# Kernel tuning notes

Measured on AMD Instinct MI355X. Metric: run time of the kernel, lower is better.

The kernel has to match this reference:

```python
import jax, jax.numpy as jnp
import numpy as np

B, S, F = 8, 2048, 256
NUM_HEADS, HEAD_DIM = 8, 64
PROJ = NUM_HEADS * HEAD_DIM


def setup_inputs() -> dict:
    key = jax.random.key(0)
    ks = jax.random.split(key, 5)
    scale = 1.0 / np.sqrt(F)
    return {
        "x": jax.random.normal(ks[0], (B, S, F), dtype=jnp.float32),
        "Wq": jax.random.normal(ks[1], (F, PROJ), dtype=jnp.float32) * scale,
        "Wk": jax.random.normal(ks[2], (F, PROJ), dtype=jnp.float32) * scale,
        "Wv": jax.random.normal(ks[3], (F, PROJ), dtype=jnp.float32) * scale,
        "Wo": jax.random.normal(ks[4], (PROJ, F), dtype=jnp.float32) * (1.0 / np.sqrt(PROJ)),
        "bo": jnp.zeros((F,), dtype=jnp.float32),
    }


def _split_heads(t):
    # [B, S, PROJ] -> [B, H, S, D]
    b, s, _ = t.shape
    return t.reshape(b, s, NUM_HEADS, HEAD_DIM).transpose(0, 2, 1, 3)


def reference(x, Wq, Wk, Wv, Wo, bo):
    q = _split_heads(x @ Wq)  # [B,H,S,D]
    k = _split_heads(x @ Wk)
    v = _split_heads(x @ Wv)

    scale = jnp.sqrt(jnp.asarray(HEAD_DIM, dtype=x.dtype))
    score = jnp.einsum("bhqd,bhkd->bhqk", q, k) / scale  # [B,H,S,S]

    # additive causal mask: -1e9 above the diagonal (matches tf band_part trick)
    s = x.shape[1]
    neg = (1.0 - jnp.tril(jnp.ones((s, s), dtype=x.dtype))) * -1e9
    score = score + neg[None, None, :, :]

    weights = jax.nn.softmax(score, axis=-1)
    attn = jnp.einsum("bhqk,bhkd->bhqd", weights, v)  # [B,H,S,D]
    concat = attn.transpose(0, 2, 1, 3).reshape(x.shape[0], s, PROJ)
    out = concat @ Wo + bo  # [B,S,F]
    return out[:, -1, :]  # keep only last sequence position
```

## Files before the change

kernel.cpp:

```cpp
#include <hip/hip_runtime.h>

#define BB 8
#define SS 2048
#define FF 256
#define HH 8
#define DD 64
#define PROJ 512
#define NCHUNK 32
#define CHUNK (SS / NCHUNK)

__global__ void __launch_bounds__(256) k_qr(
    const float* __restrict__ x, const float* __restrict__ Wq,
    const float* __restrict__ Wk, float* __restrict__ r) {
    const int b = blockIdx.x / HH;
    const int h = blockIdx.x % HH;
    const int t = threadIdx.x;
    __shared__ float xrow[FF];
    __shared__ float qp[4][DD];
    __shared__ float qh[DD];

    xrow[t] = x[((size_t)b * SS + (SS - 1)) * FF + t];
    __syncthreads();

    {
        const int g = t >> 6, d = t & 63;
        float acc = 0.f;
        const float* wqp = Wq + (size_t)(g * 64) * PROJ + h * DD + d;
#pragma unroll 8
        for (int j = 0; j < 64; ++j)
            acc += xrow[g * 64 + j] * wqp[(size_t)j * PROJ];
        qp[g][d] = acc;
    }
    __syncthreads();
    if (t < DD) qh[t] = qp[0][t] + qp[1][t] + qp[2][t] + qp[3][t];
    __syncthreads();

    const float4* wk4 = reinterpret_cast<const float4*>(Wk + (size_t)t * PROJ + h * DD);
    float acc = 0.f;
#pragma unroll
    for (int d4 = 0; d4 < DD / 4; ++d4) {
        float4 w = wk4[d4];
        acc += w.x * qh[d4 * 4 + 0] + w.y * qh[d4 * 4 + 1] +
               w.z * qh[d4 * 4 + 2] + w.w * qh[d4 * 4 + 3];
    }
    r[(size_t)blockIdx.x * FF + t] = acc * 0.125f;
}

__global__ void __launch_bounds__(512) k_chunks(
    const float* __restrict__ x, const float* __restrict__ r,
    float* __restrict__ ycp, float* __restrict__ lpart) {
    const int b = blockIdx.x / NCHUNK;
    const int c = blockIdx.x % NCHUNK;
    const int t = threadIdx.x;
    __shared__ float rl[HH][FF + 4];
    __shared__ float es[HH][CHUNK + 4];
    __shared__ float yp[2][HH][FF];

    for (int i = t; i < HH * FF; i += 512)
        rl[i >> 8][i & 255] = r[(size_t)b * HH * FF + i];
    __syncthreads();

    {
        const int sl = t >> 3, h = t & 7;
        const float4* xp = reinterpret_cast<const float4*>(
            x + ((size_t)b * SS + c * CHUNK + sl) * FF);
        const float* rp = rl[h];
        float acc = 0.f;
#pragma unroll 8
        for (int f4 = 0; f4 < FF / 4; ++f4) {
            float4 xv = xp[f4];
            acc += xv.x * rp[f4 * 4 + 0] + xv.y * rp[f4 * 4 + 1] +
                   xv.z * rp[f4 * 4 + 2] + xv.w * rp[f4 * 4 + 3];
        }
        es[h][sl] = __expf(acc);
    }
    __syncthreads();

    {
        const int h = t >> 6, ln = t & 63;
        float l = es[h][ln];
#pragma unroll
        for (int off = 32; off; off >>= 1) l += __shfl_xor(l, off);
        if (ln == 0) lpart[((size_t)(b * NCHUNK + c)) * HH + h] = l;
    }

    {
        const int f = t & 255, half = t >> 8;
        float acc[HH] = {0, 0, 0, 0, 0, 0, 0, 0};
        const float* xp = x + ((size_t)b * SS + c * CHUNK + half * 32) * FF + f;
        for (int s = 0; s < 32; ++s) {
            const float xv = xp[(size_t)s * FF];
            const int sl = half * 32 + s;
#pragma unroll
            for (int h = 0; h < HH; ++h) acc[h] += es[h][sl] * xv;
        }
#pragma unroll
        for (int h = 0; h < HH; ++h) yp[half][h][f] = acc[h];
    }
    __syncthreads();

    for (int i = t; i < HH * FF; i += 512) {
        const int h = i >> 8, f = i & 255;
        ycp[((size_t)(b * NCHUNK + c) * HH + h) * FF + f] =
            yp[0][h][f] + yp[1][h][f];
    }
}

__global__ void __launch_bounds__(256) k_comb2(
    const float* __restrict__ ycp, const float* __restrict__ lpart,
    const float* __restrict__ Wv, float* __restrict__ attn_g) {
    const int b = blockIdx.x / HH;
    const int h = blockIdx.x % HH;
    const int t = threadIdx.x;
    __shared__ float yt[FF];
    __shared__ float atl[4][DD];
    __shared__ float Linv;

    if (t < 64) {
        float l = (t < NCHUNK) ? lpart[((size_t)(b * NCHUNK + t)) * HH + h] : 0.f;
#pragma unroll
        for (int off = 32; off; off >>= 1) l += __shfl_xor(l, off);
        if (t == 0) Linv = 1.f / l;
    }

    {
        float acc = 0.f;
        const float* yb = ycp + ((size_t)(b * NCHUNK) * HH + h) * FF + t;
#pragma unroll 8
        for (int c = 0; c < NCHUNK; ++c)
            acc += yb[(size_t)c * HH * FF];
        yt[t] = acc;
    }
    __syncthreads();

    {
        const int q = t >> 6, d = t & 63;
        float acc = 0.f;
        const float* wvp = Wv + (size_t)(q * 64) * PROJ + h * DD + d;
#pragma unroll 8
        for (int j = 0; j < 64; ++j)
            acc += yt[q * 64 + j] * wvp[(size_t)j * PROJ];
        atl[q][d] = acc;
    }
    __syncthreads();

    if (t < DD) {
        attn_g[(size_t)b * PROJ + h * DD + t] =
            (atl[0][t] + atl[1][t] + atl[2][t] + atl[3][t]) * Linv;
    }
}

__global__ void __launch_bounds__(256) k_out(
    const float* __restrict__ attn_g, const float* __restrict__ Wo,
    const float* __restrict__ bo, float* __restrict__ out) {
    const int b  = blockIdx.x >> 3;
    const int fs = blockIdx.x & 7;
    const int t  = threadIdx.x;
    __shared__ float al[PROJ];
    __shared__ float po[8][32];

    for (int i = t; i < PROJ; i += 256) al[i] = attn_g[(size_t)b * PROJ + i];
    __syncthreads();

    {
        const int j = t & 31, pg = t >> 5;
        float acc = 0.f;
        const float* wop = Wo + (size_t)(pg * 64) * FF + fs * 32 + j;
        const float* ap = al + pg * 64;
#pragma unroll 8
        for (int p = 0; p < 64; ++p)
            acc += ap[p] * wop[(size_t)p * FF];
        po[pg][j] = acc;
    }
    __syncthreads();

    if (t < 32) {
        float o = bo[fs * 32 + t];
#pragma unroll
        for (int pg = 0; pg < 8; ++pg) o += po[pg][t];
        out[(size_t)b * FF + fs * 32 + t] = o;
    }
}

extern "C" void kernel_launch(void* const* d_in, const int* in_sizes, int n_in,
                              void* d_out, int out_size, void* d_ws, size_t ws_size,
                              hipStream_t stream) {
    const float* x  = (const float*)d_in[0];
    const float* Wq = (const float*)d_in[1];
    const float* Wk = (const float*)d_in[2];
    const float* Wv = (const float*)d_in[3];
    const float* Wo = (const float*)d_in[4];
    const float* bo = (const float*)d_in[5];
    float* out = (float*)d_out;

    float* ws     = (float*)d_ws;
    float* r      = ws;
    float* ycp    = r + BB * HH * FF;
    float* lpart  = ycp + (size_t)BB * NCHUNK * HH * FF;
    float* attn_g = lpart + BB * NCHUNK * HH;

    k_qr<<<BB * HH, 256, 0, stream>>>(x, Wq, Wk, r);
    k_chunks<<<BB * NCHUNK, 512, 0, stream>>>(x, r, ycp, lpart);
    k_comb2<<<BB * HH, 256, 0, stream>>>(ycp, lpart, Wv, attn_g);
    k_out<<<BB * 8, 256, 0, stream>>>(attn_g, Wo, bo, out);
}
```

Measured before the change: 31.15 us.

## Fuse chunk-combine, V projection and output projection into one tail kernel

Merges the k_comb2 and k_out kernels into a single k_tail kernel. Each block now redundantly sums all heads' chunk partials, applies the softmax normalisation, does the full Wv projection for all heads, and then computes its slice of the Wo projection. This drops one kernel launch and the attn_g global round trip. In exchange, each of the 8 blocks per batch repeats the ycp reduction and the Wv work, which adds global reads and serial compute per block.

```diff
diff --git a/kernel.cpp b/kernel.cpp
--- a/kernel.cpp
+++ b/kernel.cpp
@@ -106,69 +106,57 @@
     }
 }
 
-__global__ void __launch_bounds__(256) k_comb2(
+__global__ void __launch_bounds__(512) k_tail(
     const float* __restrict__ ycp, const float* __restrict__ lpart,
-    const float* __restrict__ Wv, float* __restrict__ attn_g) {
-    const int b = blockIdx.x / HH;
-    const int h = blockIdx.x % HH;
-    const int t = threadIdx.x;
-    __shared__ float yt[FF];
-    __shared__ float atl[4][DD];
-    __shared__ float Linv;
+    const float* __restrict__ Wv, const float* __restrict__ Wo,
+    const float* __restrict__ bo, float* __restrict__ out) {
+    const int b  = blockIdx.x >> 3;
+    const int fs = blockIdx.x & 7;
+    const int t  = threadIdx.x;
+    __shared__ float Linv[HH];
+    __shared__ float ys[HH * FF];
+    __shared__ float at[PROJ];
+    __shared__ float po[16][32];
 
-    if (t < 64) {
-        float l = (t < NCHUNK) ? lpart[((size_t)(b * NCHUNK + t)) * HH + h] : 0.f;
+    if (t < 256) {
+        const int h = t >> 5, c = t & 31;
+        float l = lpart[((size_t)(b * NCHUNK + c)) * HH + h];
 #pragma unroll
-        for (int off = 32; off; off >>= 1) l += __shfl_xor(l, off);
-        if (t == 0) Linv = 1.f / l;
+        for (int off = 16; off; off >>= 1) l += __shfl_xor(l, off);
+        if (c == 0) Linv[h] = 1.f / l;
     }
+    __syncthreads();
 
-    {
+    for (int i = t; i < HH * FF; i += 512) {
+        const int h = i >> 8, f = i & 255;
+        const float* yb = ycp + ((size_t)(b * NCHUNK) * HH + h) * FF + f;
         float acc = 0.f;
-        const float* yb = ycp + ((size_t)(b * NCHUNK) * HH + h) * FF + t;
 #pragma unroll 8
         for (int c = 0; c < NCHUNK; ++c)
             acc += yb[(size_t)c * HH * FF];
-        yt[t] = acc;
+        ys[i] = acc * Linv[h];
     }
     __syncthreads();
 
     {
-        const int q = t >> 6, d = t & 63;
+        const int h = t >> 6, d = t & 63;
         float acc = 0.f;
-        const float* wvp = Wv + (size_t)(q * 64) * PROJ + h * DD + d;
+        const float* wvp = Wv + h * DD + d;
+        const float* yh = ys + h * FF;
 #pragma unroll 8
-        for (int j = 0; j < 64; ++j)
-            acc += yt[q * 64 + j] * wvp[(size_t)j * PROJ];
-        atl[q][d] = acc;
+        for (int f = 0; f < FF; ++f)
+            acc += yh[f] * wvp[(size_t)f * PROJ];
+        at[t] = acc;
     }
-    __syncthreads();
-
-    if (t < DD) {
-        attn_g[(size_t)b * PROJ + h * DD + t] =
-            (atl[0][t] + atl[1][t] + atl[2][t] + atl[3][t]) * Linv;
-    }
-}
-
-__global__ void __launch_bounds__(256) k_out(
-    const float* __restrict__ attn_g, const float* __restrict__ Wo,
-    const float* __restrict__ bo, float* __restrict__ out) {
-    const int b  = blockIdx.x >> 3;
-    const int fs = blockIdx.x & 7;
-    const int t  = threadIdx.x;
-    __shared__ float al[PROJ];
-    __shared__ float po[8][32];
-
-    for (int i = t; i < PROJ; i += 256) al[i] = attn_g[(size_t)b * PROJ + i];
     __syncthreads();
 
     {
         const int j = t & 31, pg = t >> 5;
         float acc = 0.f;
-        const float* wop = Wo + (size_t)(pg * 64) * FF + fs * 32 + j;
-        const float* ap = al + pg * 64;
+        const float* wop = Wo + (size_t)(pg * 32) * FF + fs * 32 + j;
+        const float* ap = at + pg * 32;
 #pragma unroll 8
-        for (int p = 0; p < 64; ++p)
+        for (int p = 0; p < 32; ++p)
             acc += ap[p] * wop[(size_t)p * FF];
         po[pg][j] = acc;
     }
@@ -177,7 +165,7 @@
     if (t < 32) {
         float o = bo[fs * 32 + t];
 #pragma unroll
-        for (int pg = 0; pg < 8; ++pg) o += po[pg][t];
+        for (int pg = 0; pg < 16; ++pg) o += po[pg][t];
         out[(size_t)b * FF + fs * 32 + t] = o;
     }
 }
@@ -193,14 +181,12 @@
     const float* bo = (const float*)d_in[5];
     float* out = (float*)d_out;
 
-    float* ws     = (float*)d_ws;
-    float* r      = ws;
-    float* ycp    = r + BB * HH * FF;
-    float* lpart  = ycp + (size_t)BB * NCHUNK * HH * FF;
-    float* attn_g = lpart + BB * NCHUNK * HH;
+    float* ws    = (float*)d_ws;
+    float* r     = ws;
+    float* ycp   = r + BB * HH * FF;
+    float* lpart = ycp + (size_t)BB * NCHUNK * HH * FF;
 
     k_qr<<<BB * HH, 256, 0, stream>>>(x, Wq, Wk, r);
     k_chunks<<<BB * NCHUNK, 512, 0, stream>>>(x, r, ycp, lpart);
-    k_comb2<<<BB * HH, 256, 0, stream>>>(ycp, lpart, Wv, attn_g);
-    k_out<<<BB * 8, 256, 0, stream>>>(attn_g, Wo, bo, out);
+    k_tail<<<BB * 8, 512, 0, stream>>>(ycp, lpart, Wv, Wo, bo, out);
 }
```

Result: slower. 40.94 us (+31.4%).

## Widen parallelism across all four attention kernels with more chunks and threads

Applied to the files above, without the earlier changes.

Doubles the number of sequence chunks so k_chunks launches more blocks. It also splits the score dot product across two threads per (row, head) pair, with an extra reduction through shared memory before the exp. k_qr and k_comb2 move to 512 threads with eight-way split reductions, and k_out uses 16 feature slices per batch. The aim is to fill more compute units on a small, latency-bound problem. In exchange it writes twice as many partial outputs to workspace for k_comb2 to reduce, and adds an extra barrier.

```diff
diff --git a/kernel.cpp b/kernel.cpp
--- a/kernel.cpp
+++ b/kernel.cpp
@@ -6,44 +6,52 @@
 #define HH 8
 #define DD 64
 #define PROJ 512
-#define NCHUNK 32
+#define NCHUNK 64
 #define CHUNK (SS / NCHUNK)
 
-__global__ void __launch_bounds__(256) k_qr(
+__global__ void __launch_bounds__(512) k_qr(
     const float* __restrict__ x, const float* __restrict__ Wq,
     const float* __restrict__ Wk, float* __restrict__ r) {
     const int b = blockIdx.x / HH;
     const int h = blockIdx.x % HH;
     const int t = threadIdx.x;
     __shared__ float xrow[FF];
-    __shared__ float qp[4][DD];
+    __shared__ float qp[8][DD];
     __shared__ float qh[DD];
 
-    xrow[t] = x[((size_t)b * SS + (SS - 1)) * FF + t];
+    if (t < FF) xrow[t] = x[((size_t)b * SS + (SS - 1)) * FF + t];
     __syncthreads();
 
     {
         const int g = t >> 6, d = t & 63;
         float acc = 0.f;
-        const float* wqp = Wq + (size_t)(g * 64) * PROJ + h * DD + d;
-#pragma unroll 8
-        for (int j = 0; j < 64; ++j)
-            acc += xrow[g * 64 + j] * wqp[(size_t)j * PROJ];
+        const float* wqp = Wq + (size_t)(g * 32) * PROJ + h * DD + d;
+#pragma unroll 8
+        for (int j = 0; j < 32; ++j)
+            acc += xrow[g * 32 + j] * wqp[(size_t)j * PROJ];
         qp[g][d] = acc;
     }
     __syncthreads();
-    if (t < DD) qh[t] = qp[0][t] + qp[1][t] + qp[2][t] + qp[3][t];
-    __syncthreads();
-
-    const float4* wk4 = reinterpret_cast<const float4*>(Wk + (size_t)t * PROJ + h * DD);
-    float acc = 0.f;
-#pragma unroll
-    for (int d4 = 0; d4 < DD / 4; ++d4) {
-        float4 w = wk4[d4];
-        acc += w.x * qh[d4 * 4 + 0] + w.y * qh[d4 * 4 + 1] +
-               w.z * qh[d4 * 4 + 2] + w.w * qh[d4 * 4 + 3];
-    }
-    r[(size_t)blockIdx.x * FF + t] = acc * 0.125f;
+    if (t < DD) {
+        float q = 0.f;
+#pragma unroll
+        for (int g = 0; g < 8; ++g) q += qp[g][t];
+        qh[t] = q;
+    }
+    __syncthreads();
+
+    if (t < FF) {
+        const float4* wk4 =
+            reinterpret_cast<const float4*>(Wk + (size_t)t * PROJ + h * DD);
+        float acc = 0.f;
+#pragma unroll
+        for (int d4 = 0; d4 < DD / 4; ++d4) {
+            float4 w = wk4[d4];
+            acc += w.x * qh[d4 * 4 + 0] + w.y * qh[d4 * 4 + 1] +
+                   w.z * qh[d4 * 4 + 2] + w.w * qh[d4 * 4 + 3];
+        }
+        r[(size_t)blockIdx.x * FF + t] = acc * 0.125f;
+    }
 }
 
 __global__ void __launch_bounds__(512) k_chunks(
@@ -53,6 +61,7 @@
     const int c = blockIdx.x % NCHUNK;
     const int t = threadIdx.x;
     __shared__ float rl[HH][FF + 4];
+    __shared__ float esp[512];
     __shared__ float es[HH][CHUNK + 4];
     __shared__ float yp[2][HH][FF];
 
@@ -61,36 +70,43 @@
     __syncthreads();
 
     {
-        const int sl = t >> 3, h = t & 7;
+        const int fh = t & 1, h = (t >> 1) & 7, sl = t >> 4;
         const float4* xp = reinterpret_cast<const float4*>(
-            x + ((size_t)b * SS + c * CHUNK + sl) * FF);
-        const float* rp = rl[h];
-        float acc = 0.f;
-#pragma unroll 8
-        for (int f4 = 0; f4 < FF / 4; ++f4) {
+            x + ((size_t)b * SS + c * CHUNK + sl) * FF + fh * 128);
+        const float* rp = rl[h] + fh * 128;
+        float acc = 0.f;
+#pragma unroll 8
+        for (int f4 = 0; f4 < 32; ++f4) {
             float4 xv = xp[f4];
             acc += xv.x * rp[f4 * 4 + 0] + xv.y * rp[f4 * 4 + 1] +
                    xv.z * rp[f4 * 4 + 2] + xv.w * rp[f4 * 4 + 3];
         }
-        es[h][sl] = __expf(acc);
+        esp[t] = acc;
     }
     __syncthreads();
 
     {
         const int h = t >> 6, ln = t & 63;
-        float l = es[h][ln];
+        float l = 0.f;
+        if (ln < CHUNK) {
+            const float v = esp[ln * 16 + h * 2 + 0] + esp[ln * 16 + h * 2 + 1];
+            const float e = __expf(v);
+            es[h][ln] = e;
+            l = e;
+        }
 #pragma unroll
         for (int off = 32; off; off >>= 1) l += __shfl_xor(l, off);
         if (ln == 0) lpart[((size_t)(b * NCHUNK + c)) * HH + h] = l;
     }
+    __syncthreads();
 
     {
         const int f = t & 255, half = t >> 8;
         float acc[HH] = {0, 0, 0, 0, 0, 0, 0, 0};
-        const float* xp = x + ((size_t)b * SS + c * CHUNK + half * 32) * FF + f;
-        for (int s = 0; s < 32; ++s) {
+        const float* xp = x + ((size_t)b * SS + c * CHUNK + half * 16) * FF + f;
+        for (int s = 0; s < 16; ++s) {
             const float xv = xp[(size_t)s * FF];
-            const int sl = half * 32 + s;
+            const int sl = half * 16 + s;
 #pragma unroll
             for (int h = 0; h < HH; ++h) acc[h] += es[h][sl] * xv;
         }
@@ -106,79 +122,83 @@
     }
 }
 
-__global__ void __launch_bounds__(256) k_comb2(
+__global__ void __launch_bounds__(512) k_comb2(
     const float* __restrict__ ycp, const float* __restrict__ lpart,
     const float* __restrict__ Wv, float* __restrict__ attn_g) {
     const int b = blockIdx.x / HH;
     const int h = blockIdx.x % HH;
     const int t = threadIdx.x;
     __shared__ float yt[FF];
-    __shared__ float atl[4][DD];
+    __shared__ float atl[8][DD];
     __shared__ float Linv;
 
     if (t < 64) {
-        float l = (t < NCHUNK) ? lpart[((size_t)(b * NCHUNK + t)) * HH + h] : 0.f;
+        float l = lpart[((size_t)(b * NCHUNK + t)) * HH + h];
 #pragma unroll
         for (int off = 32; off; off >>= 1) l += __shfl_xor(l, off);
         if (t == 0) Linv = 1.f / l;
     }
 
-    {
-        float acc = 0.f;
+    if (t < FF) {
+        float a0 = 0.f, a1 = 0.f;
         const float* yb = ycp + ((size_t)(b * NCHUNK) * HH + h) * FF + t;
 #pragma unroll 8
-        for (int c = 0; c < NCHUNK; ++c)
-            acc += yb[(size_t)c * HH * FF];
-        yt[t] = acc;
-    }
-    __syncthreads();
-
-    {
-        const int q = t >> 6, d = t & 63;
-        float acc = 0.f;
-        const float* wvp = Wv + (size_t)(q * 64) * PROJ + h * DD + d;
-#pragma unroll 8
-        for (int j = 0; j < 64; ++j)
-            acc += yt[q * 64 + j] * wvp[(size_t)j * PROJ];
-        atl[q][d] = acc;
+        for (int c = 0; c < NCHUNK; c += 2) {
+            a0 += yb[(size_t)c * HH * FF];
+            a1 += yb[(size_t)(c + 1) * HH * FF];
+        }
+        yt[t] = a0 + a1;
+    }
+    __syncthreads();
+
+    {
+        const int q8 = t >> 6, d = t & 63;
+        float acc = 0.f;
+        const float* wvp = Wv + (size_t)(q8 * 32) * PROJ + h * DD + d;
+#pragma unroll 8
+        for (int j = 0; j < 32; ++j)
+            acc += yt[q8 * 32 + j] * wvp[(size_t)j * PROJ];
+        atl[q8][d] = acc;
     }
     __syncthreads();
 
     if (t < DD) {
-        attn_g[(size_t)b * PROJ + h * DD + t] =
-            (atl[0][t] + atl[1][t] + atl[2][t] + atl[3][t]) * Linv;
+        float acc = 0.f;
+#pragma unroll
+        for (int q8 = 0; q8 < 8; ++q8) acc += atl[q8][t];
+        attn_g[(size_t)b * PROJ + h * DD + t] = acc * Linv;
     }
 }
 
 __global__ void __launch_bounds__(256) k_out(
     const float* __restrict__ attn_g, const float* __restrict__ Wo,
     const float* __restrict__ bo, float* __restrict__ out) {
-    const int b  = blockIdx.x >> 3;
-    const int fs = blockIdx.x & 7;
+    const int b  = blockIdx.x >> 4;
+    const int fs = blockIdx.x & 15;
     const int t  = threadIdx.x;
     __shared__ float al[PROJ];
-    __shared__ float po[8][32];
+    __shared__ float po[16][16];
 
     for (int i = t; i < PROJ; i += 256) al[i] = attn_g[(size_t)b * PROJ + i];
     __syncthreads();
 
     {
-        const int j = t & 31, pg = t >> 5;
-        float acc = 0.f;
-        const float* wop = Wo + (size_t)(pg * 64) * FF + fs * 32 + j;
-        const float* ap = al + pg * 64;
-#pragma unroll 8
-        for (int p = 0; p < 64; ++p)
+        const int j = t & 15, pg = t >> 4;
+        float acc = 0.f;
+        const float* wop = Wo + (size_t)(pg * 32) * FF + fs * 16 + j;
+        const float* ap = al + pg * 32;
+#pragma unroll 8
+        for (int p = 0; p < 32; ++p)
             acc += ap[p] * wop[(size_t)p * FF];
         po[pg][j] = acc;
     }
     __syncthreads();
 
-    if (t < 32) {
-        float o = bo[fs * 32 + t];
-#pragma unroll
-        for (int pg = 0; pg < 8; ++pg) o += po[pg][t];
-        out[(size_t)b * FF + fs * 32 + t] = o;
+    if (t < 16) {
+        float o = bo[fs * 16 + t];
+#pragma unroll
+        for (int pg = 0; pg < 16; ++pg) o += po[pg][t];
+        out[(size_t)b * FF + fs * 16 + t] = o;
     }
 }
 
@@ -199,8 +219,8 @@
     float* lpart  = ycp + (size_t)BB * NCHUNK * HH * FF;
     float* attn_g = lpart + BB * NCHUNK * HH;
 
-    k_qr<<<BB * HH, 256, 0, stream>>>(x, Wq, Wk, r);
+    k_qr<<<BB * HH, 512, 0, stream>>>(x, Wq, Wk, r);
     k_chunks<<<BB * NCHUNK, 512, 0, stream>>>(x, r, ycp, lpart);
-    k_comb2<<<BB * HH, 256, 0, stream>>>(ycp, lpart, Wv, attn_g);
-    k_out<<<BB * 8, 256, 0, stream>>>(attn_g, Wo, bo, out);
-}
+    k_comb2<<<BB * HH, 512, 0, stream>>>(ycp, lpart, Wv, attn_g);
+    k_out<<<BB * 16, 256, 0, stream>>>(attn_g, Wo, bo, out);
+}
```

New measurement: 36.13 us. +16.0%, slower.

## Stage x chunk tiles in shared memory and reuse for scores and weighted sum

Applied to the files above, without the earlier changes.

k_chunks now loads each 32-row half of its x chunk into LDS once with coalesced float4 loads. Both the score dot products (split across two feature halves per thread) and the exp-weighted accumulation read from that tile instead of reading x twice from global memory. This cuts global traffic on x, but adds about 33KB of LDS and extra barriers per half, which may lower occupancy.

```diff
diff --git a/kernel.cpp b/kernel.cpp
--- a/kernel.cpp
+++ b/kernel.cpp
@@ -53,28 +53,60 @@
     const int c = blockIdx.x % NCHUNK;
     const int t = threadIdx.x;
     __shared__ float rl[HH][FF + 4];
+    __shared__ float xs[32][FF + 4];
+    __shared__ float esp[32][17];
     __shared__ float es[HH][CHUNK + 4];
     __shared__ float yp[2][HH][FF];
 
     for (int i = t; i < HH * FF; i += 512)
         rl[i >> 8][i & 255] = r[(size_t)b * HH * FF + i];
-    __syncthreads();
-
-    {
-        const int sl = t >> 3, h = t & 7;
-        const float4* xp = reinterpret_cast<const float4*>(
-            x + ((size_t)b * SS + c * CHUNK + sl) * FF);
-        const float* rp = rl[h];
-        float acc = 0.f;
-#pragma unroll 8
-        for (int f4 = 0; f4 < FF / 4; ++f4) {
-            float4 xv = xp[f4];
-            acc += xv.x * rp[f4 * 4 + 0] + xv.y * rp[f4 * 4 + 1] +
-                   xv.z * rp[f4 * 4 + 2] + xv.w * rp[f4 * 4 + 3];
-        }
-        es[h][sl] = __expf(acc);
-    }
-    __syncthreads();
+
+    float acc[HH] = {0, 0, 0, 0, 0, 0, 0, 0};
+    const int sub = t >> 8, f = t & 255;
+    const int p1_sl = t >> 4, p1_h = (t >> 1) & 7, p1_fh = t & 1;
+
+    for (int half = 0; half < 2; ++half) {
+        __syncthreads();
+        {
+            const float4* xg = reinterpret_cast<const float4*>(
+                x + ((size_t)b * SS + c * CHUNK + half * 32) * FF);
+            for (int i = t; i < 32 * 64; i += 512) {
+                const int sl = i >> 6, f4 = i & 63;
+                float4 v = xg[(size_t)sl * 64 + f4];
+                float* xr = &xs[sl][f4 * 4];
+                xr[0] = v.x; xr[1] = v.y; xr[2] = v.z; xr[3] = v.w;
+            }
+        }
+        __syncthreads();
+
+        {
+            const float4* xr4 =
+                reinterpret_cast<const float4*>(&xs[p1_sl][p1_fh * 128]);
+            const float* rp = rl[p1_h] + p1_fh * 128;
+            float a = 0.f;
+#pragma unroll 8
+            for (int f4 = 0; f4 < 32; ++f4) {
+                float4 xv = xr4[f4];
+                a += xv.x * rp[f4 * 4 + 0] + xv.y * rp[f4 * 4 + 1] +
+                     xv.z * rp[f4 * 4 + 2] + xv.w * rp[f4 * 4 + 3];
+            }
+            esp[p1_sl][p1_h * 2 + p1_fh] = a;
+        }
+        __syncthreads();
+
+        if (t < 256) {
+            const int h = t >> 5, ln = t & 31;
+            es[h][half * 32 + ln] = __expf(esp[ln][h * 2] + esp[ln][h * 2 + 1]);
+        }
+        __syncthreads();
+
+        for (int s = 0; s < 16; ++s) {
+            const float xv = xs[sub * 16 + s][f];
+            const int sl = half * 32 + sub * 16 + s;
+#pragma unroll
+            for (int h = 0; h < HH; ++h) acc[h] += es[h][sl] * xv;
+        }
+    }
 
     {
         const int h = t >> 6, ln = t & 63;
@@ -84,25 +116,13 @@
         if (ln == 0) lpart[((size_t)(b * NCHUNK + c)) * HH + h] = l;
     }
 
-    {
-        const int f = t & 255, half = t >> 8;
-        float acc[HH] = {0, 0, 0, 0, 0, 0, 0, 0};
-        const float* xp = x + ((size_t)b * SS + c * CHUNK + half * 32) * FF + f;
-        for (int s = 0; s < 32; ++s) {
-            const float xv = xp[(size_t)s * FF];
-            const int sl = half * 32 + s;
-#pragma unroll
-            for (int h = 0; h < HH; ++h) acc[h] += es[h][sl] * xv;
-        }
-#pragma unroll
-        for (int h = 0; h < HH; ++h) yp[half][h][f] = acc[h];
-    }
-    __syncthreads();
-
+#pragma unroll
+    for (int h = 0; h < HH; ++h) yp[sub][h][f] = acc[h];
+    __syncthreads();
     for (int i = t; i < HH * FF; i += 512) {
-        const int h = i >> 8, f = i & 255;
-        ycp[((size_t)(b * NCHUNK + c) * HH + h) * FF + f] =
-            yp[0][h][f] + yp[1][h][f];
+        const int h = i >> 8, ff = i & 255;
+        ycp[((size_t)(b * NCHUNK + c) * HH + h) * FF + ff] =
+            yp[0][h][ff] + yp[1][h][ff];
     }
 }
 
```

Result: slower. 40.04 us (+28.5%).
